# Kernel tuning notes

Measured on AMD Instinct MI355X. Metric: run time of the kernel, lower is better.

Reference implementation:

```python
import jax, jax.numpy as jnp
import numpy as np

EPS = 1e-12

def sage_layer(x, src, dst, Wl, Wr, b, n_nodes):
    # mean aggregation of source-node features into destination nodes
    msgs = x[src]                                            # [E, F] gather
    s = jax.ops.segment_sum(msgs, dst, num_segments=n_nodes)  # [N, F]
    cnt = jax.ops.segment_sum(jnp.ones((src.shape[0],), x.dtype), dst, num_segments=n_nodes)
    agg = s / jnp.maximum(cnt, 1.0)[:, None]                 # mean; 0 for isolated nodes
    out = agg @ Wl + b + x @ Wr                              # lin_l(agg) + lin_r(x_i)
    norm = jnp.linalg.norm(out, axis=-1, keepdims=True)      # normalize=True -> L2 norm
    return out / jnp.maximum(norm, EPS)


def setup_inputs() -> dict:
    key = jax.random.key(0)
    ks = jax.random.split(key, 8)
    N, E, F = 100000, 1200000, 64
    H1, H2, OUT = 64, 32, 10  # hidden_channels//2, hidden_channels//4, output_dim
    x = jax.random.normal(ks[0], (N, F), dtype=jnp.float32)
    edge_index = jax.random.randint(ks[1], (2, E), 0, N, dtype=jnp.int64)
    def glorot(k, fin, fout):
        lim = np.sqrt(6.0 / (fin + fout)).astype(np.float32)
        return jax.random.uniform(k, (fin, fout), jnp.float32, -lim, lim)
    return {
        "x": x,
        "edge_index": edge_index,
        "W1l": glorot(ks[2], F, H1), "W1r": glorot(ks[3], F, H1), "b1": jnp.zeros((H1,), jnp.float32),
        "W2l": glorot(ks[4], H1, H2), "W2r": glorot(ks[5], H1, H2), "b2": jnp.zeros((H2,), jnp.float32),
        "W3l": glorot(ks[6], H2, OUT), "W3r": glorot(ks[7], H2, OUT), "b3": jnp.zeros((OUT,), jnp.float32),
    }


def reference(x, edge_index, W1l, W1r, b1, W2l, W2r, b2, W3l, W3r, b3):
    n = x.shape[0]
    src, dst = edge_index[0], edge_index[1]
    h = jax.nn.relu(sage_layer(x, src, dst, W1l, W1r, b1, n))
    h = jax.nn.relu(sage_layer(h, src, dst, W2l, W2r, b2, n))
    h = sage_layer(h, src, dst, W3l, W3r, b3, n)
    return jax.nn.log_softmax(h, axis=1)
```

## Files before the change

kernel.cpp:

```cpp
#include <hip/hip_runtime.h>
#include <math.h>


typedef __attribute__((ext_vector_type(8))) short short8;
typedef __attribute__((ext_vector_type(4))) float floatx4;
typedef __attribute__((ext_vector_type(2))) float floatx2;

__device__ __forceinline__ unsigned short f2bf(float f) {
    unsigned u = __float_as_uint(f);
    u += 0x7fffu + ((u >> 16) & 1u);
    return (unsigned short)(u >> 16);
}
__device__ __forceinline__ float blo(unsigned u) { return __uint_as_float(u << 16); }
__device__ __forceinline__ float bhi(unsigned u) { return __uint_as_float(u & 0xffff0000u); }
__device__ __forceinline__ unsigned char f2fp8(float f) {
    return (unsigned char)(__builtin_amdgcn_cvt_pk_fp8_f32(f, f, 0, false) & 0xFF);
}


__global__ __launch_bounds__(256) void hist_kernel(
        const int* __restrict__ ei, int* __restrict__ bh, int E, int NB, int NBKT) {
    __shared__ int lh[256];
    const int tid = threadIdx.x, blk = blockIdx.x;
    lh[tid] = 0;
    __syncthreads();
    const int base = blk << 12;
#pragma unroll
    for (int i = 0; i < 16; ++i) {
        const int e = base + (i << 8) + tid;
        if (e < E) atomicAdd(&lh[min((int)(((unsigned)ei[E + e]) >> 9), NBKT - 1)], 1);
    }
    __syncthreads();
    if (tid < NBKT) bh[tid * NB + blk] = lh[tid];
}

__global__ __launch_bounds__(256) void bscan_kernel(
        const int* __restrict__ bh, int* __restrict__ offs, int* __restrict__ btot,
        int NB, int NBKT) {
    const int lane = threadIdx.x & 63;
    const int w = blockIdx.x * 4 + (threadIdx.x >> 6);
    if (w >= NBKT) return;
    int running = 0;
    for (int base = 0; base < NB; base += 64) {
        const int j = base + lane;
        const int v = (j < NB) ? bh[w * NB + j] : 0;
        int incl = v;
#pragma unroll
        for (int off = 1; off < 64; off <<= 1) {
            const int t = __shfl_up(incl, off);
            if (lane >= off) incl += t;
        }
        if (j < NB) offs[w * NB + j] = running + incl - v;
        running += __shfl(incl, 63);
    }
    if (lane == 0) btot[w] = running;
}

__global__ __launch_bounds__(64) void bucketbase_kernel(
        const int* __restrict__ btot, int* __restrict__ bucket_base, int NBKT) {
    const int lane = threadIdx.x;
    int running = 0;
    for (int base = 0; base < NBKT; base += 64) {
        const int j = base + lane;
        const int v = (j < NBKT) ? btot[j] : 0;
        int incl = v;
#pragma unroll
        for (int off = 1; off < 64; off <<= 1) {
            const int t = __shfl_up(incl, off);
            if (lane >= off) incl += t;
        }
        if (j < NBKT) bucket_base[j] = running + incl - v;
        running += __shfl(incl, 63);
    }
    if (lane == 0) bucket_base[NBKT] = running;
}

__global__ __launch_bounds__(256) void scatter_kernel(
        const int* __restrict__ ei, const int* __restrict__ offs,
        const int* __restrict__ bucket_base, unsigned* __restrict__ ebuf,
        int E, int NB, int NBKT) {
    __shared__ int lcur[256];
    const int tid = threadIdx.x, blk = blockIdx.x;
    if (tid < NBKT) lcur[tid] = bucket_base[tid] + offs[tid * NB + blk];
    __syncthreads();
    const int base = blk << 12;
#pragma unroll
    for (int i = 0; i < 16; ++i) {
        const int e = base + (i << 8) + tid;
        if (e < E) {
            const int s = ei[e];
            const unsigned d = (unsigned)ei[E + e];
            int p = atomicAdd(&lcur[min((int)(d >> 9), NBKT - 1)], 1);
            p = min(p, E - 1);
            ebuf[p] = ((d & 511u) << 17) | (unsigned)s;
        }
    }
}

__global__ __launch_bounds__(512) void bucket_csr_kernel(
        const unsigned* __restrict__ ebuf, const int* __restrict__ bucket_base,
        int* __restrict__ rowptr, int* __restrict__ deg, int* __restrict__ col,
        int N, int E, int half) {
    __shared__ int ldeg[512];
    __shared__ int ldeg_lo[512];
    __shared__ int buf[512];
    __shared__ int lcur_lo[512];
    __shared__ int lcur_hi[512];
    const int b = blockIdx.x, tid = threadIdx.x;
    const int segbase = bucket_base[b];
    const int L = bucket_base[b + 1] - segbase;
    ldeg[tid] = 0; ldeg_lo[tid] = 0;
    __syncthreads();
    for (int i = tid; i < L; i += 512) {
        const unsigned p = ebuf[segbase + i];
        const int ln = p >> 17;
        atomicAdd(&ldeg[ln], 1);
        if ((int)(p & 0x1FFFFu) < half) atomicAdd(&ldeg_lo[ln], 1);
    }
    __syncthreads();
    buf[tid] = ldeg[tid];
    __syncthreads();
    for (int off = 1; off < 512; off <<= 1) {
        const int t = (tid >= off) ? buf[tid - off] : 0;
        __syncthreads();
        buf[tid] += t;
        __syncthreads();
    }
    const int excl = buf[tid] - ldeg[tid];
    const int node = (b << 9) + tid;
    if (node < N) { rowptr[node] = segbase + excl; deg[node] = ldeg[tid]; }
    lcur_lo[tid] = excl;
    lcur_hi[tid] = excl + ldeg_lo[tid];
    __syncthreads();
    for (int i = tid; i < L; i += 512) {
        const unsigned p = ebuf[segbase + i];
        const int ln = p >> 17;
        const int s  = (int)(p & 0x1FFFFu);
        int pos = (s < half) ? atomicAdd(&lcur_lo[ln], 1) : atomicAdd(&lcur_hi[ln], 1);
        pos = min(segbase + pos, E - 1);
        col[pos] = s;
    }
}

template <int K, int F_OUT, int PAD, bool AFP32, bool YL8>
__global__ __launch_bounds__(256) void transform_kernel(
        const void* __restrict__ Ain, const float* __restrict__ Wl,
        const float* __restrict__ Wr, const float* __restrict__ b,
        void* __restrict__ yl, unsigned short* __restrict__ yr, int n) {
    constexpr int KSTEP = K / 32;
    constexpr int NT = PAD / 16;
    const int lane = threadIdx.x & 63;
    const int wid = (blockIdx.x * blockDim.x + threadIdx.x) >> 6;
    const int ntiles = (n + 15) >> 4;
    if (wid >= ntiles) return;
    const int nl = lane & 15, q = lane >> 4;

    short8 Bl[NT][KSTEP], Br[NT][KSTEP];
    float biasv[NT];
#pragma unroll
    for (int t = 0; t < NT; ++t) {
        const int ncol = t * 16 + nl;
        biasv[t] = (ncol < F_OUT) ? b[ncol] : 0.f;
#pragma unroll
        for (int ks = 0; ks < KSTEP; ++ks) {
#pragma unroll
            for (int j = 0; j < 8; ++j) {
                const int k = ks * 32 + q * 8 + j;
                Bl[t][ks][j] = (ncol < F_OUT) ? (short)f2bf(Wl[k * F_OUT + ncol]) : (short)0;
                Br[t][ks][j] = (ncol < F_OUT) ? (short)f2bf(Wr[k * F_OUT + ncol]) : (short)0;
            }
        }
    }

    const int m0 = wid * 16;
    int m = m0 + nl; if (m >= n) m = n - 1;

    short8 a[KSTEP];
#pragma unroll
    for (int ks = 0; ks < KSTEP; ++ks) {
        if (AFP32) {
            const float* p = (const float*)Ain + (size_t)m * K + ks * 32 + q * 8;
#pragma unroll
            for (int j = 0; j < 8; ++j) a[ks][j] = (short)f2bf(p[j]);
        } else {
            union { uint4 u; short8 s; } cvt;
            cvt.u = *(const uint4*)((const unsigned short*)Ain + (size_t)m * K + ks * 32 + q * 8);
            a[ks] = cvt.s;
        }
    }

    floatx4 accl[NT], accr[NT];
#pragma unroll
    for (int t = 0; t < NT; ++t) { accl[t] = {0.f,0.f,0.f,0.f}; accr[t] = {0.f,0.f,0.f,0.f}; }
#pragma unroll
    for (int ks = 0; ks < KSTEP; ++ks) {
#pragma unroll
        for (int t = 0; t < NT; ++t) {
            accl[t] = __builtin_amdgcn_mfma_f32_16x16x32_bf16(a[ks], Bl[t][ks], accl[t], 0, 0, 0);
            accr[t] = __builtin_amdgcn_mfma_f32_16x16x32_bf16(a[ks], Br[t][ks], accr[t], 0, 0, 0);
        }
    }

#pragma unroll
    for (int t = 0; t < NT; ++t) {
        const int ncol = t * 16 + nl;
#pragma unroll
        for (int r = 0; r < 4; ++r) {
            const int node = m0 + q * 4 + r;
            if (node < n) {
                if (YL8)
                    ((unsigned char*)yl)[(size_t)node * PAD + ncol] = f2fp8(accl[t][r]);
                else
                    ((unsigned short*)yl)[(size_t)node * PAD + ncol] = f2bf(accl[t][r]);
                yr[(size_t)node * PAD + ncol] = f2bf(accr[t][r] + biasv[t]);
            }
        }
    }
}

template <int F, int ACT, int PK>
__global__ __launch_bounds__(256) void agg_kernel(
        const void* __restrict__ yl, const unsigned short* __restrict__ yr,
        const int* __restrict__ rowptr, const int* __restrict__ degv,
        const int* __restrict__ col,
        unsigned short* __restrict__ hout, float* __restrict__ fout, int n) {
    constexpr int G = F / 8;
    constexpr int NPW = 64 / G;
    const int lane = threadIdx.x & 63;
    const int wid = (blockIdx.x * blockDim.x + threadIdx.x) >> 6;
    const int g = lane / G, c = lane % G;
    const int node = wid * NPW + g;
    if (node >= n) return;

    const int beg = rowptr[node];
    const int dg  = degv[node];
    const int nmax = n - 1;

    float a0=0.f,a1=0.f,a2=0.f,a3=0.f,a4=0.f,a5=0.f,a6=0.f,a7=0.f;
    int i = 0;
    if (PK == 1) {
        const unsigned char* base = (const unsigned char*)yl + c * 8;
        auto accrow = [&](uint2 t) {
            const floatx2 p0 = __builtin_amdgcn_cvt_pk_f32_fp8((int)t.x, false);
            const floatx2 p1 = __builtin_amdgcn_cvt_pk_f32_fp8((int)t.x, true);
            const floatx2 p2 = __builtin_amdgcn_cvt_pk_f32_fp8((int)t.y, false);
            const floatx2 p3 = __builtin_amdgcn_cvt_pk_f32_fp8((int)t.y, true);
            a0 += p0.x; a1 += p0.y; a2 += p1.x; a3 += p1.y;
            a4 += p2.x; a5 += p2.y; a6 += p3.x; a7 += p3.y;
        };
        for (; i + 4 <= dg; i += 4) {
            const int n0 = min(col[beg + i],     nmax);
            const int n1 = min(col[beg + i + 1], nmax);
            const int n2 = min(col[beg + i + 2], nmax);
            const int n3 = min(col[beg + i + 3], nmax);
            const uint2 t0 = *(const uint2*)(base + (size_t)n0 * F);
            const uint2 t1 = *(const uint2*)(base + (size_t)n1 * F);
            const uint2 t2 = *(const uint2*)(base + (size_t)n2 * F);
            const uint2 t3 = *(const uint2*)(base + (size_t)n3 * F);
            accrow(t0); accrow(t1); accrow(t2); accrow(t3);
        }
        for (; i < dg; ++i) {
            const int n0 = min(col[beg + i], nmax);
            accrow(*(const uint2*)(base + (size_t)n0 * F));
        }
    } else {
        const unsigned short* base = (const unsigned short*)yl + c * 8;
        for (; i + 4 <= dg; i += 4) {
            const int n0 = min(col[beg + i],     nmax);
            const int n1 = min(col[beg + i + 1], nmax);
            const int n2 = min(col[beg + i + 2], nmax);
            const int n3 = min(col[beg + i + 3], nmax);
            const uint4 t0 = *(const uint4*)(base + (size_t)n0 * F);
            const uint4 t1 = *(const uint4*)(base + (size_t)n1 * F);
            const uint4 t2 = *(const uint4*)(base + (size_t)n2 * F);
            const uint4 t3 = *(const uint4*)(base + (size_t)n3 * F);
            a0 += blo(t0.x) + blo(t1.x) + blo(t2.x) + blo(t3.x);
            a1 += bhi(t0.x) + bhi(t1.x) + bhi(t2.x) + bhi(t3.x);
            a2 += blo(t0.y) + blo(t1.y) + blo(t2.y) + blo(t3.y);
            a3 += bhi(t0.y) + bhi(t1.y) + bhi(t2.y) + bhi(t3.y);
            a4 += blo(t0.z) + blo(t1.z) + blo(t2.z) + blo(t3.z);
            a5 += bhi(t0.z) + bhi(t1.z) + bhi(t2.z) + bhi(t3.z);
            a6 += blo(t0.w) + blo(t1.w) + blo(t2.w) + blo(t3.w);
            a7 += bhi(t0.w) + bhi(t1.w) + bhi(t2.w) + bhi(t3.w);
        }
        for (; i < dg; ++i) {
            const int n0 = min(col[beg + i], nmax);
            const uint4 t0 = *(const uint4*)(base + (size_t)n0 * F);
            a0 += blo(t0.x); a1 += bhi(t0.x); a2 += blo(t0.y); a3 += bhi(t0.y);
            a4 += blo(t0.z); a5 += bhi(t0.z); a6 += blo(t0.w); a7 += bhi(t0.w);
        }
    }
    const float inv = (dg > 0) ? 1.f / (float)dg : 0.f;

    const uint4 rv = *(const uint4*)(yr + (size_t)node * F + c * 8);
    float o[8];
    o[0] = a0*inv + blo(rv.x); o[1] = a1*inv + bhi(rv.x);
    o[2] = a2*inv + blo(rv.y); o[3] = a3*inv + bhi(rv.y);
    o[4] = a4*inv + blo(rv.z); o[5] = a5*inv + bhi(rv.z);
    o[6] = a6*inv + blo(rv.w); o[7] = a7*inv + bhi(rv.w);

    float ss = 0.f;
#pragma unroll
    for (int j = 0; j < 8; ++j) ss += o[j] * o[j];
#pragma unroll
    for (int off = 1; off < G; off <<= 1) ss += __shfl_xor(ss, off);
    const float scale = 1.f / fmaxf(sqrtf(ss), 1e-12f);

    if (ACT == 1) {
        uint4 u;
        float h[8];
#pragma unroll
        for (int j = 0; j < 8; ++j) h[j] = fmaxf(o[j] * scale, 0.f);
        u.x = (unsigned)f2bf(h[0]) | ((unsigned)f2bf(h[1]) << 16);
        u.y = (unsigned)f2bf(h[2]) | ((unsigned)f2bf(h[3]) << 16);
        u.z = (unsigned)f2bf(h[4]) | ((unsigned)f2bf(h[5]) << 16);
        u.w = (unsigned)f2bf(h[6]) | ((unsigned)f2bf(h[7]) << 16);
        *(uint4*)(hout + (size_t)node * F + c * 8) = u;
    } else {
#pragma unroll
        for (int j = 0; j < 8; ++j) o[j] *= scale;
        const int cbase = c * 8;
        float m = -INFINITY;
#pragma unroll
        for (int j = 0; j < 8; ++j) if (cbase + j < 10) m = fmaxf(m, o[j]);
        m = fmaxf(m, __shfl_xor(m, 1));
        float s = 0.f;
#pragma unroll
        for (int j = 0; j < 8; ++j) if (cbase + j < 10) s += __expf(o[j] - m);
        s += __shfl_xor(s, 1);
        const float ls = logf(s);
#pragma unroll
        for (int j = 0; j < 8; ++j)
            if (cbase + j < 10) fout[(size_t)node * 10 + cbase + j] = o[j] - m - ls;
    }
}

extern "C" void kernel_launch(void* const* d_in, const int* in_sizes, int n_in,
                              void* d_out, int out_size, void* d_ws, size_t ws_size,
                              hipStream_t stream) {
    const float* x   = (const float*)d_in[0];
    const int*   ei  = (const int*)d_in[1];
    const float* W1l = (const float*)d_in[2];
    const float* W1r = (const float*)d_in[3];
    const float* b1  = (const float*)d_in[4];
    const float* W2l = (const float*)d_in[5];
    const float* W2r = (const float*)d_in[6];
    const float* b2  = (const float*)d_in[7];
    const float* W3l = (const float*)d_in[8];
    const float* W3r = (const float*)d_in[9];
    const float* b3  = (const float*)d_in[10];
    float*       out = (float*)d_out;

    const int N = in_sizes[0] / 64;
    const int E = in_sizes[1] / 2;
    const int NBKT = (N + 511) >> 9;
    const int NB   = (E + 4095) >> 12;

    auto align16 = [](size_t v) { return (v + 15) & ~(size_t)15; };
    char* ws = (char*)d_ws;
    size_t off = 0;
    int* rowptr  = (int*)(ws + off); off = align16(off + (size_t)N * 4);
    int* deg     = (int*)(ws + off); off = align16(off + (size_t)N * 4);
    int* colidx  = (int*)(ws + off); off = align16(off + (size_t)E * 4);
    unsigned* ebuf = (unsigned*)(ws + off); off = align16(off + (size_t)E * 4);
    int* bh      = (int*)(ws + off); off = align16(off + (size_t)NBKT * NB * 4);
    int* offsb   = (int*)(ws + off); off = align16(off + (size_t)NBKT * NB * 4);
    int* btot    = (int*)(ws + off); off = align16(off + (size_t)NBKT * 4);
    int* bbase   = (int*)(ws + off); off = align16(off + (size_t)(NBKT + 1) * 4);
    unsigned char*  y1l = (unsigned char*)(ws + off);  off = align16(off + (size_t)N * 64);
    unsigned short* y1r = (unsigned short*)(ws + off); off = align16(off + (size_t)N * 64 * 2);
    unsigned short* h1  = (unsigned short*)(ws + off); off = align16(off + (size_t)N * 64 * 2);
    unsigned char*  y2l = (unsigned char*)(ws + off);  off = align16(off + (size_t)N * 32);
    unsigned short* y2r = (unsigned short*)(ws + off); off = align16(off + (size_t)N * 32 * 2);
    unsigned short* h2  = (unsigned short*)(ws + off); off = align16(off + (size_t)N * 32 * 2);
    unsigned short* y3l = (unsigned short*)(ws + off); off = align16(off + (size_t)N * 16 * 2);
    unsigned short* y3r = (unsigned short*)(ws + off); off = align16(off + (size_t)N * 16 * 2);
    (void)ws_size; (void)n_in; (void)out_size;

    hist_kernel<<<NB, 256, 0, stream>>>(ei, bh, E, NB, NBKT);
    bscan_kernel<<<(NBKT + 3) / 4, 256, 0, stream>>>(bh, offsb, btot, NB, NBKT);
    bucketbase_kernel<<<1, 64, 0, stream>>>(btot, bbase, NBKT);
    scatter_kernel<<<NB, 256, 0, stream>>>(ei, offsb, bbase, ebuf, E, NB, NBKT);
    bucket_csr_kernel<<<NBKT, 512, 0, stream>>>(ebuf, bbase, rowptr, deg, colidx, N, E, N / 2);

    const int ntiles = (N + 15) / 16;
    const int tblocks = (ntiles * 64 + 255) / 256;

    transform_kernel<64, 64, 64, true, true><<<tblocks, 256, 0, stream>>>(
        x, W1l, W1r, b1, y1l, y1r, N);
    agg_kernel<64, 1, 1><<<(N + 31) / 32, 256, 0, stream>>>(
        y1l, y1r, rowptr, deg, colidx, h1, nullptr, N);
    transform_kernel<64, 32, 32, false, true><<<tblocks, 256, 0, stream>>>(
        h1, W2l, W2r, b2, y2l, y2r, N);
    agg_kernel<32, 1, 1><<<(N + 63) / 64, 256, 0, stream>>>(
        y2l, y2r, rowptr, deg, colidx, h2, nullptr, N);
    transform_kernel<32, 10, 16, false, false><<<tblocks, 256, 0, stream>>>(
        h2, W3l, W3r, b3, y3l, y3r, N);
    agg_kernel<16, 2, 0><<<(N + 127) / 128, 256, 0, stream>>>(
        y3l, y3r, rowptr, deg, colidx, nullptr, out, N);
}
```

Measured before the change: 213.2 us.

## Split each node's neighbor gather across eight lane groups with shuffle reduction

The aggregation kernel now gives each destination node eight edge-lanes times G feature-lanes instead of G lanes. Each edge-lane walks a strided slice of the neighbor list, and the partial sums are combined with xor shuffles. This exposes more independent gathers per node and evens out load across nodes of different degree, at the cost of eight times more waves, extra shuffles, and idle lanes when degrees are small (average about 12). Writes are limited to the e==0 lanes, and out-of-range nodes are masked rather than returning early.

```diff
diff --git a/kernel.cpp b/kernel.cpp
--- a/kernel.cpp
+++ b/kernel.cpp
@@ -224,75 +224,56 @@
         const int* __restrict__ rowptr, const int* __restrict__ degv,
         const int* __restrict__ col,
         unsigned short* __restrict__ hout, float* __restrict__ fout, int n) {
-    constexpr int G = F / 8;
-    constexpr int NPW = 64 / G;
+    constexpr int G   = F / 8;
+    constexpr int EPN = 8;
+    constexpr int LPN = G * EPN;
+    constexpr int NPW = 64 / LPN;
     const int lane = threadIdx.x & 63;
-    const int wid = (blockIdx.x * blockDim.x + threadIdx.x) >> 6;
-    const int g = lane / G, c = lane % G;
-    const int node = wid * NPW + g;
-    if (node >= n) return;
-
-    const int beg = rowptr[node];
-    const int dg  = degv[node];
+    const int wid  = (blockIdx.x * blockDim.x + threadIdx.x) >> 6;
+    const int sub  = lane / LPN;
+    const int l    = lane % LPN;
+    const int e    = l / G;
+    const int c    = l % G;
+    const int node = wid * NPW + sub;
+    const bool valid = node < n;
+
+    const int beg = valid ? rowptr[node] : 0;
+    const int dg  = valid ? degv[node] : 0;
     const int nmax = n - 1;
 
     float a0=0.f,a1=0.f,a2=0.f,a3=0.f,a4=0.f,a5=0.f,a6=0.f,a7=0.f;
-    int i = 0;
-    if (PK == 1) {
-        const unsigned char* base = (const unsigned char*)yl + c * 8;
-        auto accrow = [&](uint2 t) {
-            const floatx2 p0 = __builtin_amdgcn_cvt_pk_f32_fp8((int)t.x, false);
-            const floatx2 p1 = __builtin_amdgcn_cvt_pk_f32_fp8((int)t.x, true);
-            const floatx2 p2 = __builtin_amdgcn_cvt_pk_f32_fp8((int)t.y, false);
-            const floatx2 p3 = __builtin_amdgcn_cvt_pk_f32_fp8((int)t.y, true);
-            a0 += p0.x; a1 += p0.y; a2 += p1.x; a3 += p1.y;
-            a4 += p2.x; a5 += p2.y; a6 += p3.x; a7 += p3.y;
-        };
-        for (; i + 4 <= dg; i += 4) {
-            const int n0 = min(col[beg + i],     nmax);
-            const int n1 = min(col[beg + i + 1], nmax);
-            const int n2 = min(col[beg + i + 2], nmax);
-            const int n3 = min(col[beg + i + 3], nmax);
-            const uint2 t0 = *(const uint2*)(base + (size_t)n0 * F);
-            const uint2 t1 = *(const uint2*)(base + (size_t)n1 * F);
-            const uint2 t2 = *(const uint2*)(base + (size_t)n2 * F);
-            const uint2 t3 = *(const uint2*)(base + (size_t)n3 * F);
-            accrow(t0); accrow(t1); accrow(t2); accrow(t3);
-        }
-        for (; i < dg; ++i) {
-            const int n0 = min(col[beg + i], nmax);
-            accrow(*(const uint2*)(base + (size_t)n0 * F));
-        }
-    } else {
-        const unsigned short* base = (const unsigned short*)yl + c * 8;
-        for (; i + 4 <= dg; i += 4) {
-            const int n0 = min(col[beg + i],     nmax);
-            const int n1 = min(col[beg + i + 1], nmax);
-            const int n2 = min(col[beg + i + 2], nmax);
-            const int n3 = min(col[beg + i + 3], nmax);
-            const uint4 t0 = *(const uint4*)(base + (size_t)n0 * F);
-            const uint4 t1 = *(const uint4*)(base + (size_t)n1 * F);
-            const uint4 t2 = *(const uint4*)(base + (size_t)n2 * F);
-            const uint4 t3 = *(const uint4*)(base + (size_t)n3 * F);
-            a0 += blo(t0.x) + blo(t1.x) + blo(t2.x) + blo(t3.x);
-            a1 += bhi(t0.x) + bhi(t1.x) + bhi(t2.x) + bhi(t3.x);
-            a2 += blo(t0.y) + blo(t1.y) + blo(t2.y) + blo(t3.y);
-            a3 += bhi(t0.y) + bhi(t1.y) + bhi(t2.y) + bhi(t3.y);
-            a4 += blo(t0.z) + blo(t1.z) + blo(t2.z) + blo(t3.z);
-            a5 += bhi(t0.z) + bhi(t1.z) + bhi(t2.z) + bhi(t3.z);
-            a6 += blo(t0.w) + blo(t1.w) + blo(t2.w) + blo(t3.w);
-            a7 += bhi(t0.w) + bhi(t1.w) + bhi(t2.w) + bhi(t3.w);
-        }
-        for (; i < dg; ++i) {
-            const int n0 = min(col[beg + i], nmax);
-            const uint4 t0 = *(const uint4*)(base + (size_t)n0 * F);
-            a0 += blo(t0.x); a1 += bhi(t0.x); a2 += blo(t0.y); a3 += bhi(t0.y);
-            a4 += blo(t0.z); a5 += bhi(t0.z); a6 += blo(t0.w); a7 += bhi(t0.w);
-        }
-    }
+    for (int base = 0; base < dg; base += EPN) {
+        const int idx = base + e;
+        if (idx < dg) {
+            const int r = min(col[beg + idx], nmax);
+            if (PK == 1) {
+                const uint2 t = *(const uint2*)((const unsigned char*)yl + (size_t)r * F + c * 8);
+                const floatx2 p0 = __builtin_amdgcn_cvt_pk_f32_fp8((int)t.x, false);
+                const floatx2 p1 = __builtin_amdgcn_cvt_pk_f32_fp8((int)t.x, true);
+                const floatx2 p2 = __builtin_amdgcn_cvt_pk_f32_fp8((int)t.y, false);
+                const floatx2 p3 = __builtin_amdgcn_cvt_pk_f32_fp8((int)t.y, true);
+                a0 += p0.x; a1 += p0.y; a2 += p1.x; a3 += p1.y;
+                a4 += p2.x; a5 += p2.y; a6 += p3.x; a7 += p3.y;
+            } else {
+                const uint4 t = *(const uint4*)((const unsigned short*)yl + (size_t)r * F + c * 8);
+                a0 += blo(t.x); a1 += bhi(t.x); a2 += blo(t.y); a3 += bhi(t.y);
+                a4 += blo(t.z); a5 += bhi(t.z); a6 += blo(t.w); a7 += bhi(t.w);
+            }
+        }
+    }
+
+#pragma unroll
+    for (int off = G; off < LPN; off <<= 1) {
+        a0 += __shfl_xor(a0, off); a1 += __shfl_xor(a1, off);
+        a2 += __shfl_xor(a2, off); a3 += __shfl_xor(a3, off);
+        a4 += __shfl_xor(a4, off); a5 += __shfl_xor(a5, off);
+        a6 += __shfl_xor(a6, off); a7 += __shfl_xor(a7, off);
+    }
+
     const float inv = (dg > 0) ? 1.f / (float)dg : 0.f;
 
-    const uint4 rv = *(const uint4*)(yr + (size_t)node * F + c * 8);
+    uint4 rv = {0u, 0u, 0u, 0u};
+    if (valid) rv = *(const uint4*)(yr + (size_t)node * F + c * 8);
     float o[8];
     o[0] = a0*inv + blo(rv.x); o[1] = a1*inv + bhi(rv.x);
     o[2] = a2*inv + blo(rv.y); o[3] = a3*inv + bhi(rv.y);
@@ -307,15 +288,17 @@
     const float scale = 1.f / fmaxf(sqrtf(ss), 1e-12f);
 
     if (ACT == 1) {
-        uint4 u;
-        float h[8];
-#pragma unroll
-        for (int j = 0; j < 8; ++j) h[j] = fmaxf(o[j] * scale, 0.f);
-        u.x = (unsigned)f2bf(h[0]) | ((unsigned)f2bf(h[1]) << 16);
-        u.y = (unsigned)f2bf(h[2]) | ((unsigned)f2bf(h[3]) << 16);
-        u.z = (unsigned)f2bf(h[4]) | ((unsigned)f2bf(h[5]) << 16);
-        u.w = (unsigned)f2bf(h[6]) | ((unsigned)f2bf(h[7]) << 16);
-        *(uint4*)(hout + (size_t)node * F + c * 8) = u;
+        if (valid && e == 0) {
+            uint4 u;
+            float h[8];
+#pragma unroll
+            for (int j = 0; j < 8; ++j) h[j] = fmaxf(o[j] * scale, 0.f);
+            u.x = (unsigned)f2bf(h[0]) | ((unsigned)f2bf(h[1]) << 16);
+            u.y = (unsigned)f2bf(h[2]) | ((unsigned)f2bf(h[3]) << 16);
+            u.z = (unsigned)f2bf(h[4]) | ((unsigned)f2bf(h[5]) << 16);
+            u.w = (unsigned)f2bf(h[6]) | ((unsigned)f2bf(h[7]) << 16);
+            *(uint4*)(hout + (size_t)node * F + c * 8) = u;
+        }
     } else {
 #pragma unroll
         for (int j = 0; j < 8; ++j) o[j] *= scale;
@@ -329,9 +312,11 @@
         for (int j = 0; j < 8; ++j) if (cbase + j < 10) s += __expf(o[j] - m);
         s += __shfl_xor(s, 1);
         const float ls = logf(s);
-#pragma unroll
-        for (int j = 0; j < 8; ++j)
-            if (cbase + j < 10) fout[(size_t)node * 10 + cbase + j] = o[j] - m - ls;
+        if (valid && e == 0) {
+#pragma unroll
+            for (int j = 0; j < 8; ++j)
+                if (cbase + j < 10) fout[(size_t)node * 10 + cbase + j] = o[j] - m - ls;
+        }
     }
 }
 
@@ -386,16 +371,21 @@
     const int ntiles = (N + 15) / 16;
     const int tblocks = (ntiles * 64 + 255) / 256;
 
+    auto aggblocks = [](int n, int npw) {
+        const int waves = (n + npw - 1) / npw;
+        return (waves + 3) / 4;
+    };
+
     transform_kernel<64, 64, 64, true, true><<<tblocks, 256, 0, stream>>>(
         x, W1l, W1r, b1, y1l, y1r, N);
-    agg_kernel<64, 1, 1><<<(N + 31) / 32, 256, 0, stream>>>(
+    agg_kernel<64, 1, 1><<<aggblocks(N, 1), 256, 0, stream>>>(
         y1l, y1r, rowptr, deg, colidx, h1, nullptr, N);
     transform_kernel<64, 32, 32, false, true><<<tblocks, 256, 0, stream>>>(
         h1, W2l, W2r, b2, y2l, y2r, N);
-    agg_kernel<32, 1, 1><<<(N + 63) / 64, 256, 0, stream>>>(
+    agg_kernel<32, 1, 1><<<aggblocks(N, 2), 256, 0, stream>>>(
         y2l, y2r, rowptr, deg, colidx, h2, nullptr, N);
     transform_kernel<32, 10, 16, false, false><<<tblocks, 256, 0, stream>>>(
         h2, W3l, W3r, b3, y3l, y3r, N);
-    agg_kernel<16, 2, 0><<<(N + 127) / 128, 256, 0, stream>>>(
+    agg_kernel<16, 2, 0><<<aggblocks(N, 4), 256, 0, stream>>>(
         y3l, y3r, rowptr, deg, colidx, nullptr, out, N);
 }
```

Result: slower. 250.6 us (+17.6%).
